# Performance work log

Hardware: AMD Instinct MI355X
Metric: run time of the kernel (lower is better)

## Reference

```python
import jax, jax.numpy as jnp
import numpy as np

B, S, D = 8, 2048, 512
EPS = float(jnp.finfo(jnp.float32).eps)  # torch RMSNorm eps=None -> finfo eps


def rmsnorm(x, w):
    var = jnp.mean(jnp.square(x), axis=-1, keepdims=True)
    return x * jax.lax.rsqrt(var + EPS) * w


def setup_inputs() -> dict:
    key = jax.random.key(0)
    ks = jax.random.split(key, 9)
    x = jax.random.normal(ks[0], (B, S, D), dtype=jnp.float32)
    q_expl = jax.random.normal(ks[1], (B, S, D), dtype=jnp.float32)
    k_expl = jax.random.normal(ks[2], (B, S, D), dtype=jnp.float32)
    # parameters (torch Linear: y = x @ W^T + b; store W already transposed [in, out])
    sc1 = 1.0 / np.sqrt(D)
    W1 = jax.random.uniform(ks[3], (D, 2 * D), jnp.float32, -sc1, sc1)
    b1 = jax.random.uniform(ks[4], (2 * D,), jnp.float32, -sc1, sc1)
    W2 = jax.random.uniform(ks[5], (D, D), jnp.float32, -sc1, sc1)
    b2 = jax.random.uniform(ks[6], (D,), jnp.float32, -sc1, sc1)
    norm1_w = jnp.ones((D,), jnp.float32)
    norm2_w = jnp.ones((D,), jnp.float32)
    return {"x": x, "q_expl": q_expl, "k_expl": k_expl,
            "W1": W1, "b1": b1, "W2": W2, "b2": b2,
            "norm1_w": norm1_w, "norm2_w": norm2_w}


def reference(x, q_expl, k_expl, W1, b1, W2, b2, norm1_w, norm2_w):
    d = x.shape[-1]
    # single-head attention: scores [B,S,S]
    scores = jnp.einsum('bqd,bkd->bqk', q_expl, k_expl) / jnp.sqrt(jnp.float32(d))
    attn = jax.nn.softmax(scores, axis=-1)
    attn_out = jnp.einsum('bqk,bkd->bqd', attn, x)
    # dropout is identity in eval mode
    h = rmsnorm(x + attn_out, norm1_w)
    # GeGLU FFN: Linear(D->2D), chunk, gelu(x1)*x2, Linear(D->D)
    proj = h @ W1 + b1
    x1, x2 = jnp.split(proj, 2, axis=-1)
    g = jax.nn.gelu(x1, approximate=False) * x2
    ff = g @ W2 + b2
    return rmsnorm(h + ff, norm2_w)
```

## Files before the change

kernel.cpp:

```cpp
#include <hip/hip_runtime.h>
#include <math.h>

static constexpr float EPS_F = 1.1920929e-07f;
static constexpr float SCL   = 0.044194173824159216f;

typedef __attribute__((ext_vector_type(8))) short  short8;
typedef __attribute__((ext_vector_type(4))) float  floatx4;

__device__ __forceinline__ float4 ld4(const float* p){ return *(const float4*)p; }
__device__ __forceinline__ ushort f2bf(float f){
  union { float f; unsigned u; } v; v.f = f;
  return (ushort)((v.u + 0x7FFFu + ((v.u >> 16) & 1u)) >> 16);
}
__device__ __forceinline__ float bf2f(ushort h){
  union { unsigned u; float f; } v; v.u = ((unsigned)h) << 16;
  return v.f;
}
#define MFMA16(A,B,C) __builtin_amdgcn_mfma_f32_16x16x32_bf16((A),(B),(C),0,0,0)

__device__ __forceinline__ void gld16(void* lds, const void* g){
  __builtin_amdgcn_global_load_lds(
      (const __attribute__((address_space(1))) unsigned int*)g,
      (__attribute__((address_space(3))) unsigned int*)lds, 16, 0, 0);
}


__global__ __launch_bounds__(256)
void cvt_qk(const float* __restrict__ q, const float* __restrict__ k,
            ushort* __restrict__ Qb, ushort* __restrict__ Kb)
{
  const size_t i4 = ((size_t)blockIdx.x*256 + threadIdx.x)*4;
  float4 v = ld4(q + i4);
  ushort4 o;
  o.x=f2bf(v.x*SCL); o.y=f2bf(v.y*SCL); o.z=f2bf(v.z*SCL); o.w=f2bf(v.w*SCL);
  *(ushort4*)(Qb + i4) = o;
  float4 u = ld4(k + i4);
  o.x=f2bf(u.x); o.y=f2bf(u.y); o.z=f2bf(u.z); o.w=f2bf(u.w);
  *(ushort4*)(Kb + i4) = o;
}

__global__ __launch_bounds__(256)
void transpose_cvt(const float* __restrict__ in, ushort* __restrict__ out,
                   int R, int C)
{
  __shared__ __align__(16) ushort tile[64*68];
  const int t = threadIdx.x;
  const size_t boff = (size_t)blockIdx.z * R * C;
  const int c0 = blockIdx.x*64, r0 = blockIdx.y*64;
#pragma unroll
  for (int it = 0; it < 4; ++it){
    int f = t + it*256, r = f >> 4, c4 = f & 15;
    float4 v = ld4(in + boff + (size_t)(r0+r)*C + c0 + c4*4);
    ushort4 o; o.x=f2bf(v.x); o.y=f2bf(v.y); o.z=f2bf(v.z); o.w=f2bf(v.w);
    *(ushort4*)&tile[r*68 + c4*4] = o;
  }
  __syncthreads();
#pragma unroll
  for (int it = 0; it < 4; ++it){
    int f = t + it*256, c = f >> 4, q4 = f & 15;
    ushort4 o;
    o.x = tile[(q4*4+0)*68 + c];
    o.y = tile[(q4*4+1)*68 + c];
    o.z = tile[(q4*4+2)*68 + c];
    o.w = tile[(q4*4+3)*68 + c];
    *(ushort4*)(out + boff + (size_t)(c0+c)*R + r0 + q4*4) = o;
  }
}

__global__ __launch_bounds__(256)
void qk_gemm(const ushort* __restrict__ Qbf, const ushort* __restrict__ Kbf,
             ushort* __restrict__ scores)
{
  __shared__ __align__(16) ushort As[128*32];
  __shared__ __align__(16) ushort Bs[128*32];
  const int t=threadIdx.x, lane=t&63, w=t>>6;
  const int b=blockIdx.z, m0=blockIdx.y*128, n0=blockIdx.x*128;
  const ushort* Qb = Qbf + ((size_t)b*2048 + m0)*512;
  const ushort* Kb = Kbf + ((size_t)b*2048 + n0)*512;
  const int sr = w*32 + (lane>>2);
  const int sc = (lane&3)*8;
  const int ga=(w&1)*4, gb2=(w>>1)*4;
  const int l15=lane&15, quad=lane>>4;

  floatx4 acc[4][4];
#pragma unroll
  for (int i=0;i<4;++i)
#pragma unroll
    for (int j=0;j<4;++j) acc[i][j]=(floatx4){0.f,0.f,0.f,0.f};

  for (int kc=0; kc<16; ++kc){
    const int k0 = kc*32;
    gld16(&As[(w*32)*32],    Qb + (size_t)sr*512      + k0 + sc);
    gld16(&As[(w*32+16)*32], Qb + (size_t)(sr+16)*512 + k0 + sc);
    gld16(&Bs[(w*32)*32],    Kb + (size_t)sr*512      + k0 + sc);
    gld16(&Bs[(w*32+16)*32], Kb + (size_t)(sr+16)*512 + k0 + sc);
    __syncthreads();
    short8 af[4], bfr[4];
#pragma unroll
    for (int i=0;i<4;++i) af[i]  = *(const short8*)&As[((ga+i)*16 + l15)*32 + quad*8];
#pragma unroll
    for (int j=0;j<4;++j) bfr[j] = *(const short8*)&Bs[((gb2+j)*16 + l15)*32 + quad*8];
#pragma unroll
    for (int i=0;i<4;++i)
#pragma unroll
      for (int j=0;j<4;++j)
        acc[i][j] = MFMA16(af[i], bfr[j], acc[i][j]);
    __syncthreads();
  }

  ushort* sb = scores + (size_t)b*2048*2048;
#pragma unroll
  for (int i=0;i<4;++i){
    const int rm = m0 + (ga+i)*16 + quad*4;
#pragma unroll
    for (int j=0;j<4;++j){
      const int cn = n0 + (gb2+j)*16 + l15;
#pragma unroll
      for (int r=0;r<4;++r)
        sb[(size_t)(rm+r)*2048 + cn] = f2bf(acc[i][j][r]);
    }
  }
}

__global__ __launch_bounds__(256)
void softmax_rows(ushort* __restrict__ sp)
{
  __shared__ float wred[8];
  const int t = threadIdx.x;
  ushort* row = sp + ((size_t)blockIdx.y*2048 + blockIdx.x)*2048;
  ushort4 u0 = *(const ushort4*)&row[t*4];
  ushort4 u1 = *(const ushort4*)&row[1024 + t*4];
  float v[8] = {bf2f(u0.x), bf2f(u0.y), bf2f(u0.z), bf2f(u0.w),
                bf2f(u1.x), bf2f(u1.y), bf2f(u1.z), bf2f(u1.w)};
  float mx = v[0];
#pragma unroll
  for (int e=1;e<8;++e) mx = fmaxf(mx, v[e]);
#pragma unroll
  for (int s=1;s<64;s<<=1) mx = fmaxf(mx, __shfl_xor(mx, s));
  if ((t&63)==0) wred[t>>6] = mx;
  __syncthreads();
  mx = fmaxf(fmaxf(wred[0],wred[1]), fmaxf(wred[2],wred[3]));
  float sum = 0.f;
#pragma unroll
  for (int e=0;e<8;++e){ v[e] = __expf(v[e]-mx); sum += v[e]; }
#pragma unroll
  for (int s=1;s<64;s<<=1) sum += __shfl_xor(sum, s);
  if ((t&63)==0) wred[4 + (t>>6)] = sum;
  __syncthreads();
  const float is = 1.0f/(wred[4]+wred[5]+wred[6]+wred[7]);
  u0.x=f2bf(v[0]*is); u0.y=f2bf(v[1]*is); u0.z=f2bf(v[2]*is); u0.w=f2bf(v[3]*is);
  u1.x=f2bf(v[4]*is); u1.y=f2bf(v[5]*is); u1.z=f2bf(v[6]*is); u1.w=f2bf(v[7]*is);
  *(ushort4*)&row[t*4] = u0;
  *(ushort4*)&row[1024 + t*4] = u1;
}

__global__ __launch_bounds__(512)
void pv_rms1(const ushort* __restrict__ P, const ushort* __restrict__ XT,
             const float* __restrict__ x, const float* __restrict__ n1w,
             ushort* __restrict__ hbf)
{
  __shared__ __align__(16) ushort Ps[64*32];
  __shared__ __align__(16) ushort Xs[512*32];
  __shared__ float red[64*8];
  const int t=threadIdx.x, lane=t&63, w=t>>6;
  const int m0=blockIdx.x*64, b=m0>>11, lm=m0&2047;
  const ushort* Pb = P  + ((size_t)b*2048 + lm)*2048;
  const ushort* Xb = XT + (size_t)b*512*2048;
  const int srq = lane>>2, sc=(lane&3)*8;
  const int l15=lane&15, quad=lane>>4;

  floatx4 acc[4][4];
#pragma unroll
  for (int i=0;i<4;++i)
#pragma unroll
    for (int j=0;j<4;++j) acc[i][j]=(floatx4){0.f,0.f,0.f,0.f};

  for (int kc=0; kc<64; ++kc){
    const int k0 = kc*32;
    if (w < 4)
      gld16(&Ps[(w*16)*32], Pb + (size_t)(w*16+srq)*2048 + k0 + sc);
#pragma unroll
    for (int i2=0;i2<4;++i2)
      gld16(&Xs[(w*64+i2*16)*32], Xb + (size_t)(w*64+i2*16+srq)*2048 + k0 + sc);
    __syncthreads();
    short8 af[4], bfr[4];
#pragma unroll
    for (int i=0;i<4;++i) af[i]  = *(const short8*)&Ps[(i*16 + l15)*32 + quad*8];
#pragma unroll
    for (int j=0;j<4;++j) bfr[j] = *(const short8*)&Xs[((w*4+j)*16 + l15)*32 + quad*8];
#pragma unroll
    for (int i=0;i<4;++i)
#pragma unroll
      for (int j=0;j<4;++j)
        acc[i][j] = MFMA16(af[i], bfr[j], acc[i][j]);
    __syncthreads();
  }

  float part[4][4];
#pragma unroll
  for (int i=0;i<4;++i)
#pragma unroll
    for (int r=0;r<4;++r) part[i][r]=0.f;
#pragma unroll
  for (int i=0;i<4;++i)
#pragma unroll
    for (int j=0;j<4;++j){
      const int col = w*64 + j*16 + l15;
#pragma unroll
      for (int r=0;r<4;++r){
        const int row = m0 + i*16 + quad*4 + r;
        float o = acc[i][j][r] + x[(size_t)row*512 + col];
        acc[i][j][r] = o;
        part[i][r] += o*o;
      }
    }
#pragma unroll
  for (int i=0;i<4;++i)
#pragma unroll
    for (int r=0;r<4;++r){
      float p = part[i][r];
      p += __shfl_xor(p,1); p += __shfl_xor(p,2);
      p += __shfl_xor(p,4); p += __shfl_xor(p,8);
      part[i][r] = p;
    }
  if (l15 == 0){
#pragma unroll
    for (int i=0;i<4;++i)
#pragma unroll
      for (int r=0;r<4;++r)
        red[(i*16 + quad*4 + r)*8 + w] = part[i][r];
  }
  __syncthreads();
#pragma unroll
  for (int i=0;i<4;++i)
#pragma unroll
    for (int r=0;r<4;++r){
      const int lr = i*16 + quad*4 + r;
      float tot = red[lr*8]+red[lr*8+1]+red[lr*8+2]+red[lr*8+3]
                + red[lr*8+4]+red[lr*8+5]+red[lr*8+6]+red[lr*8+7];
      part[i][r] = rsqrtf(tot*(1.0f/512.0f) + EPS_F);
    }
#pragma unroll
  for (int i=0;i<4;++i)
#pragma unroll
    for (int j=0;j<4;++j){
      const int col = w*64 + j*16 + l15;
      const float wv = n1w[col];
#pragma unroll
      for (int r=0;r<4;++r){
        const int row = m0 + i*16 + quad*4 + r;
        hbf[(size_t)row*512 + col] = f2bf(acc[i][j][r] * part[i][r] * wv);
      }
    }
}

__global__ __launch_bounds__(256)
void ffn1(const ushort* __restrict__ hbf, const ushort* __restrict__ W1T,
          const float* __restrict__ b1, ushort* __restrict__ gbuf)
{
  __shared__ __align__(16) ushort As[128*32];
  __shared__ __align__(16) ushort Bs[128*32];
  const int t=threadIdx.x, lane=t&63, w=t>>6;
  const int n0=blockIdx.x*64, m0=blockIdx.y*128;
  const int sr = w*32 + (lane>>2), sc=(lane&3)*8;
  const int ga=(w&1)*4, b2=(w>>1);
  const int l15=lane&15, quad=lane>>4;
  const int gr0 = (sr < 64) ? (n0+sr) : (448+n0+sr);
  const int sr1 = sr+16;
  const int gr1 = (sr1 < 64) ? (n0+sr1) : (448+n0+sr1);

  floatx4 acc[4][4];
#pragma unroll
  for (int i=0;i<4;++i)
#pragma unroll
    for (int j=0;j<4;++j) acc[i][j]=(floatx4){0.f,0.f,0.f,0.f};

  for (int kc=0; kc<16; ++kc){
    const int k0 = kc*32;
    gld16(&As[(w*32)*32],    hbf + (size_t)(m0+sr)*512  + k0 + sc);
    gld16(&As[(w*32+16)*32], hbf + (size_t)(m0+sr1)*512 + k0 + sc);
    gld16(&Bs[(w*32)*32],    W1T + (size_t)gr0*512 + k0 + sc);
    gld16(&Bs[(w*32+16)*32], W1T + (size_t)gr1*512 + k0 + sc);
    __syncthreads();
    short8 af[4], bfr[4];
#pragma unroll
    for (int i=0;i<4;++i) af[i] = *(const short8*)&As[((ga+i)*16 + l15)*32 + quad*8];
#pragma unroll
    for (int jj=0;jj<4;++jj){
      const int g1 = (jj<2) ? (b2*2+jj) : (4 + b2*2 + (jj-2));
      bfr[jj] = *(const short8*)&Bs[(g1*16 + l15)*32 + quad*8];
    }
#pragma unroll
    for (int i=0;i<4;++i)
#pragma unroll
      for (int jj=0;jj<4;++jj)
        acc[i][jj] = MFMA16(af[i], bfr[jj], acc[i][jj]);
    __syncthreads();
  }

#pragma unroll
  for (int i=0;i<4;++i){
#pragma unroll
    for (int jj=0;jj<2;++jj){
      const int col = n0 + (b2*2+jj)*16 + l15;
      const float bb1 = b1[col], bb2 = b1[512+col];
#pragma unroll
      for (int r=0;r<4;++r){
        const int row = m0 + (ga+i)*16 + quad*4 + r;
        float x1 = acc[i][jj][r]   + bb1;
        float x2 = acc[i][jj+2][r] + bb2;
        float gl = 0.5f*x1*(1.0f + erff(x1*0.70710678118654752f));
        gbuf[(size_t)row*512 + col] = f2bf(gl*x2);
      }
    }
  }
}

__global__ __launch_bounds__(512)
void ffn2_rms2(const ushort* __restrict__ gb, const ushort* __restrict__ W2T,
               const float* __restrict__ b2, const ushort* __restrict__ hbf,
               const float* __restrict__ n2w, float* __restrict__ out)
{
  __shared__ __align__(16) ushort As[64*32];
  __shared__ __align__(16) ushort Bs[512*32];
  __shared__ float red[64*8];
  const int t=threadIdx.x, lane=t&63, w=t>>6;
  const int m0=blockIdx.x*64;
  const int srq = lane>>2, sc=(lane&3)*8;
  const int l15=lane&15, quad=lane>>4;

  floatx4 acc[4][4];
#pragma unroll
  for (int i=0;i<4;++i)
#pragma unroll
    for (int j=0;j<4;++j) acc[i][j]=(floatx4){0.f,0.f,0.f,0.f};

  for (int kc=0; kc<16; ++kc){
    const int k0 = kc*32;
    if (w < 4)
      gld16(&As[(w*16)*32], gb + (size_t)(m0+w*16+srq)*512 + k0 + sc);
#pragma unroll
    for (int i2=0;i2<4;++i2)
      gld16(&Bs[(w*64+i2*16)*32], W2T + (size_t)(w*64+i2*16+srq)*512 + k0 + sc);
    __syncthreads();
    short8 af[4], bfr[4];
#pragma unroll
    for (int i=0;i<4;++i) af[i]  = *(const short8*)&As[(i*16 + l15)*32 + quad*8];
#pragma unroll
    for (int j=0;j<4;++j) bfr[j] = *(const short8*)&Bs[((w*4+j)*16 + l15)*32 + quad*8];
#pragma unroll
    for (int i=0;i<4;++i)
#pragma unroll
      for (int j=0;j<4;++j)
        acc[i][j] = MFMA16(af[i], bfr[j], acc[i][j]);
    __syncthreads();
  }

  float part[4][4];
#pragma unroll
  for (int i=0;i<4;++i)
#pragma unroll
    for (int r=0;r<4;++r) part[i][r]=0.f;
#pragma unroll
  for (int i=0;i<4;++i)
#pragma unroll
    for (int j=0;j<4;++j){
      const int col = w*64 + j*16 + l15;
      const float bb = b2[col];
#pragma unroll
      for (int r=0;r<4;++r){
        const int row = m0 + i*16 + quad*4 + r;
        float y = acc[i][j][r] + bb + bf2f(hbf[(size_t)row*512 + col]);
        acc[i][j][r] = y;
        part[i][r] += y*y;
      }
    }
#pragma unroll
  for (int i=0;i<4;++i)
#pragma unroll
    for (int r=0;r<4;++r){
      float p = part[i][r];
      p += __shfl_xor(p,1); p += __shfl_xor(p,2);
      p += __shfl_xor(p,4); p += __shfl_xor(p,8);
      part[i][r] = p;
    }
  if (l15 == 0){
#pragma unroll
    for (int i=0;i<4;++i)
#pragma unroll
      for (int r=0;r<4;++r)
        red[(i*16 + quad*4 + r)*8 + w] = part[i][r];
  }
  __syncthreads();
#pragma unroll
  for (int i=0;i<4;++i)
#pragma unroll
    for (int r=0;r<4;++r){
      const int lr = i*16 + quad*4 + r;
      float tot = red[lr*8]+red[lr*8+1]+red[lr*8+2]+red[lr*8+3]
                + red[lr*8+4]+red[lr*8+5]+red[lr*8+6]+red[lr*8+7];
      part[i][r] = rsqrtf(tot*(1.0f/512.0f) + EPS_F);
    }
#pragma unroll
  for (int i=0;i<4;++i)
#pragma unroll
    for (int j=0;j<4;++j){
      const int col = w*64 + j*16 + l15;
      const float wv = n2w[col];
#pragma unroll
      for (int r=0;r<4;++r){
        const int row = m0 + i*16 + quad*4 + r;
        out[(size_t)row*512 + col] = acc[i][j][r] * part[i][r] * wv;
      }
    }
}

extern "C" void kernel_launch(void* const* d_in, const int* in_sizes, int n_in,
                              void* d_out, int out_size, void* d_ws, size_t ws_size,
                              hipStream_t stream)
{
  const float* x   = (const float*)d_in[0];
  const float* q   = (const float*)d_in[1];
  const float* k   = (const float*)d_in[2];
  const float* W1  = (const float*)d_in[3];
  const float* b1  = (const float*)d_in[4];
  const float* W2  = (const float*)d_in[5];
  const float* b2  = (const float*)d_in[6];
  const float* n1w = (const float*)d_in[7];
  const float* n2w = (const float*)d_in[8];
  float* out = (float*)d_out;

  ushort* scoresP = (ushort*)d_ws;
  ushort* XT  = scoresP + (size_t)8*2048*2048;
  ushort* Qbf = XT  + (size_t)8*512*2048;
  ushort* Kbf = Qbf + (size_t)8*2048*512;
  ushort* W1T = Kbf + (size_t)8*2048*512;
  ushort* W2T = W1T + (size_t)1024*512;
  ushort* hbf  = Qbf;
  ushort* gbuf = Kbf;

  cvt_qk       <<<dim3(8192),     256, 0, stream>>>(q, k, Qbf, Kbf);
  transpose_cvt<<<dim3(8, 32, 8), 256, 0, stream>>>(x,  XT,  2048, 512);
  transpose_cvt<<<dim3(16, 8, 1), 256, 0, stream>>>(W1, W1T, 512, 1024);
  transpose_cvt<<<dim3(8,  8, 1), 256, 0, stream>>>(W2, W2T, 512, 512);

  qk_gemm      <<<dim3(16, 16, 8), 256, 0, stream>>>(Qbf, Kbf, scoresP);
  softmax_rows <<<dim3(2048, 8),   256, 0, stream>>>(scoresP);
  pv_rms1      <<<dim3(256),       512, 0, stream>>>(scoresP, XT, x, n1w, hbf);
  ffn1         <<<dim3(8, 128),    256, 0, stream>>>(hbf, W1T, b1, gbuf);
  ffn2_rms2    <<<dim3(256),       512, 0, stream>>>(gbuf, W2T, b2, hbf, n2w, out);
}
```

Baseline: 365.4 us.

## Double-buffer LDS in all GEMM kernels and halve row tiles for PV/FFN2

```diff
diff --git a/kernel.cpp b/kernel.cpp
--- a/kernel.cpp
+++ b/kernel.cpp
@@ -71,16 +71,14 @@
 void qk_gemm(const ushort* __restrict__ Qbf, const ushort* __restrict__ Kbf,
              ushort* __restrict__ scores)
 {
-  __shared__ __align__(16) ushort As[128*32];
-  __shared__ __align__(16) ushort Bs[128*32];
+  __shared__ __align__(16) ushort As[2][128*32];
+  __shared__ __align__(16) ushort Bs[2][128*32];
   const int t=threadIdx.x, lane=t&63, w=t>>6;
   const int b=blockIdx.z, m0=blockIdx.y*128, n0=blockIdx.x*128;
   const ushort* Qb = Qbf + ((size_t)b*2048 + m0)*512;
   const ushort* Kb = Kbf + ((size_t)b*2048 + n0)*512;
-  const int sr = w*32 + (lane>>2);
-  const int sc = (lane&3)*8;
-  const int ga=(w&1)*4, gb2=(w>>1)*4;
-  const int l15=lane&15, quad=lane>>4;
+  const int sr = w*32 + (lane>>2), sc = (lane&3)*8;
+  const int ga=(w&1)*4, gb2=(w>>1)*4, l15=lane&15, quad=lane>>4;
 
   floatx4 acc[4][4];
 #pragma unroll
@@ -88,24 +86,29 @@
 #pragma unroll
     for (int j=0;j<4;++j) acc[i][j]=(floatx4){0.f,0.f,0.f,0.f};
 
+  auto stage = [&](int buf, int k0){
+    gld16(&As[buf][(w*32)*32],    Qb + (size_t)sr*512      + k0 + sc);
+    gld16(&As[buf][(w*32+16)*32], Qb + (size_t)(sr+16)*512 + k0 + sc);
+    gld16(&Bs[buf][(w*32)*32],    Kb + (size_t)sr*512      + k0 + sc);
+    gld16(&Bs[buf][(w*32+16)*32], Kb + (size_t)(sr+16)*512 + k0 + sc);
+  };
+
+  stage(0, 0);
   for (int kc=0; kc<16; ++kc){
-    const int k0 = kc*32;
-    gld16(&As[(w*32)*32],    Qb + (size_t)sr*512      + k0 + sc);
-    gld16(&As[(w*32+16)*32], Qb + (size_t)(sr+16)*512 + k0 + sc);
-    gld16(&Bs[(w*32)*32],    Kb + (size_t)sr*512      + k0 + sc);
-    gld16(&Bs[(w*32+16)*32], Kb + (size_t)(sr+16)*512 + k0 + sc);
     __syncthreads();
+    if (kc < 15) stage((kc+1)&1, (kc+1)*32);
+    const ushort* A = As[kc&1];
+    const ushort* B = Bs[kc&1];
     short8 af[4], bfr[4];
 #pragma unroll
-    for (int i=0;i<4;++i) af[i]  = *(const short8*)&As[((ga+i)*16 + l15)*32 + quad*8];
-#pragma unroll
-    for (int j=0;j<4;++j) bfr[j] = *(const short8*)&Bs[((gb2+j)*16 + l15)*32 + quad*8];
+    for (int i=0;i<4;++i) af[i]  = *(const short8*)&A[((ga+i)*16 + l15)*32 + quad*8];
+#pragma unroll
+    for (int j=0;j<4;++j) bfr[j] = *(const short8*)&B[((gb2+j)*16 + l15)*32 + quad*8];
 #pragma unroll
     for (int i=0;i<4;++i)
 #pragma unroll
       for (int j=0;j<4;++j)
         acc[i][j] = MFMA16(af[i], bfr[j], acc[i][j]);
-    __syncthreads();
   }
 
   ushort* sb = scores + (size_t)b*2048*2048;
@@ -159,50 +162,55 @@
              const float* __restrict__ x, const float* __restrict__ n1w,
              ushort* __restrict__ hbf)
 {
-  __shared__ __align__(16) ushort Ps[64*32];
-  __shared__ __align__(16) ushort Xs[512*32];
-  __shared__ float red[64*8];
+  __shared__ __align__(16) ushort Ps[2][32*32];
+  __shared__ __align__(16) ushort Xs[2][512*32];
+  __shared__ float red[32*8];
   const int t=threadIdx.x, lane=t&63, w=t>>6;
-  const int m0=blockIdx.x*64, b=m0>>11, lm=m0&2047;
+  const int m0=blockIdx.x*32, b=m0>>11, lm=m0&2047;
   const ushort* Pb = P  + ((size_t)b*2048 + lm)*2048;
   const ushort* Xb = XT + (size_t)b*512*2048;
   const int srq = lane>>2, sc=(lane&3)*8;
   const int l15=lane&15, quad=lane>>4;
 
-  floatx4 acc[4][4];
-#pragma unroll
-  for (int i=0;i<4;++i)
+  floatx4 acc[2][4];
+#pragma unroll
+  for (int i=0;i<2;++i)
 #pragma unroll
     for (int j=0;j<4;++j) acc[i][j]=(floatx4){0.f,0.f,0.f,0.f};
 
+  auto stage = [&](int buf, int k0){
+    if (w < 2)
+      gld16(&Ps[buf][(w*16)*32], Pb + (size_t)(w*16+srq)*2048 + k0 + sc);
+#pragma unroll
+    for (int i2=0;i2<4;++i2)
+      gld16(&Xs[buf][(w*64+i2*16)*32], Xb + (size_t)(w*64+i2*16+srq)*2048 + k0 + sc);
+  };
+
+  stage(0, 0);
   for (int kc=0; kc<64; ++kc){
-    const int k0 = kc*32;
-    if (w < 4)
-      gld16(&Ps[(w*16)*32], Pb + (size_t)(w*16+srq)*2048 + k0 + sc);
-#pragma unroll
-    for (int i2=0;i2<4;++i2)
-      gld16(&Xs[(w*64+i2*16)*32], Xb + (size_t)(w*64+i2*16+srq)*2048 + k0 + sc);
     __syncthreads();
-    short8 af[4], bfr[4];
-#pragma unroll
-    for (int i=0;i<4;++i) af[i]  = *(const short8*)&Ps[(i*16 + l15)*32 + quad*8];
-#pragma unroll
-    for (int j=0;j<4;++j) bfr[j] = *(const short8*)&Xs[((w*4+j)*16 + l15)*32 + quad*8];
-#pragma unroll
-    for (int i=0;i<4;++i)
+    if (kc < 63) stage((kc+1)&1, (kc+1)*32);
+    const ushort* A = Ps[kc&1];
+    const ushort* B = Xs[kc&1];
+    short8 af[2], bfr[4];
+#pragma unroll
+    for (int i=0;i<2;++i) af[i]  = *(const short8*)&A[(i*16 + l15)*32 + quad*8];
+#pragma unroll
+    for (int j=0;j<4;++j) bfr[j] = *(const short8*)&B[((w*4+j)*16 + l15)*32 + quad*8];
+#pragma unroll
+    for (int i=0;i<2;++i)
 #pragma unroll
       for (int j=0;j<4;++j)
         acc[i][j] = MFMA16(af[i], bfr[j], acc[i][j]);
-    __syncthreads();
-  }
-
-  float part[4][4];
-#pragma unroll
-  for (int i=0;i<4;++i)
+  }
+
+  float part[2][4];
+#pragma unroll
+  for (int i=0;i<2;++i)
 #pragma unroll
     for (int r=0;r<4;++r) part[i][r]=0.f;
 #pragma unroll
-  for (int i=0;i<4;++i)
+  for (int i=0;i<2;++i)
 #pragma unroll
     for (int j=0;j<4;++j){
       const int col = w*64 + j*16 + l15;
@@ -215,7 +223,7 @@
       }
     }
 #pragma unroll
-  for (int i=0;i<4;++i)
+  for (int i=0;i<2;++i)
 #pragma unroll
     for (int r=0;r<4;++r){
       float p = part[i][r];
@@ -225,14 +233,14 @@
     }
   if (l15 == 0){
 #pragma unroll
-    for (int i=0;i<4;++i)
+    for (int i=0;i<2;++i)
 #pragma unroll
       for (int r=0;r<4;++r)
         red[(i*16 + quad*4 + r)*8 + w] = part[i][r];
   }
   __syncthreads();
 #pragma unroll
-  for (int i=0;i<4;++i)
+  for (int i=0;i<2;++i)
 #pragma unroll
     for (int r=0;r<4;++r){
       const int lr = i*16 + quad*4 + r;
@@ -241,7 +249,7 @@
       part[i][r] = rsqrtf(tot*(1.0f/512.0f) + EPS_F);
     }
 #pragma unroll
-  for (int i=0;i<4;++i)
+  for (int i=0;i<2;++i)
 #pragma unroll
     for (int j=0;j<4;++j){
       const int col = w*64 + j*16 + l15;
@@ -258,12 +266,12 @@
 void ffn1(const ushort* __restrict__ hbf, const ushort* __restrict__ W1T,
           const float* __restrict__ b1, ushort* __restrict__ gbuf)
 {
-  __shared__ __align__(16) ushort As[128*32];
-  __shared__ __align__(16) ushort Bs[128*32];
+  __shared__ __align__(16) ushort As[2][128*32];
+  __shared__ __align__(16) ushort Bs[2][128*32];
   const int t=threadIdx.x, lane=t&63, w=t>>6;
   const int n0=blockIdx.x*64, m0=blockIdx.y*128;
   const int sr = w*32 + (lane>>2), sc=(lane&3)*8;
-  const int ga=(w&1)*4, b2=(w>>1);
+  const int ga=(w&1)*4, b2w=(w>>1);
   const int l15=lane&15, quad=lane>>4;
   const int gr0 = (sr < 64) ? (n0+sr) : (448+n0+sr);
   const int sr1 = sr+16;
@@ -275,34 +283,39 @@
 #pragma unroll
     for (int j=0;j<4;++j) acc[i][j]=(floatx4){0.f,0.f,0.f,0.f};
 
+  auto stage = [&](int buf, int k0){
+    gld16(&As[buf][(w*32)*32],    hbf + (size_t)(m0+sr)*512  + k0 + sc);
+    gld16(&As[buf][(w*32+16)*32], hbf + (size_t)(m0+sr1)*512 + k0 + sc);
+    gld16(&Bs[buf][(w*32)*32],    W1T + (size_t)gr0*512 + k0 + sc);
+    gld16(&Bs[buf][(w*32+16)*32], W1T + (size_t)gr1*512 + k0 + sc);
+  };
+
+  stage(0, 0);
   for (int kc=0; kc<16; ++kc){
-    const int k0 = kc*32;
-    gld16(&As[(w*32)*32],    hbf + (size_t)(m0+sr)*512  + k0 + sc);
-    gld16(&As[(w*32+16)*32], hbf + (size_t)(m0+sr1)*512 + k0 + sc);
-    gld16(&Bs[(w*32)*32],    W1T + (size_t)gr0*512 + k0 + sc);
-    gld16(&Bs[(w*32+16)*32], W1T + (size_t)gr1*512 + k0 + sc);
     __syncthreads();
+    if (kc < 15) stage((kc+1)&1, (kc+1)*32);
+    const ushort* A = As[kc&1];
+    const ushort* B = Bs[kc&1];
     short8 af[4], bfr[4];
 #pragma unroll
-    for (int i=0;i<4;++i) af[i] = *(const short8*)&As[((ga+i)*16 + l15)*32 + quad*8];
+    for (int i=0;i<4;++i) af[i] = *(const short8*)&A[((ga+i)*16 + l15)*32 + quad*8];
 #pragma unroll
     for (int jj=0;jj<4;++jj){
-      const int g1 = (jj<2) ? (b2*2+jj) : (4 + b2*2 + (jj-2));
-      bfr[jj] = *(const short8*)&Bs[(g1*16 + l15)*32 + quad*8];
+      const int g1 = (jj<2) ? (b2w*2+jj) : (4 + b2w*2 + (jj-2));
+      bfr[jj] = *(const short8*)&B[(g1*16 + l15)*32 + quad*8];
     }
 #pragma unroll
     for (int i=0;i<4;++i)
 #pragma unroll
       for (int jj=0;jj<4;++jj)
         acc[i][jj] = MFMA16(af[i], bfr[jj], acc[i][jj]);
-    __syncthreads();
   }
 
 #pragma unroll
   for (int i=0;i<4;++i){
 #pragma unroll
     for (int jj=0;jj<2;++jj){
-      const int col = n0 + (b2*2+jj)*16 + l15;
+      const int col = n0 + (b2w*2+jj)*16 + l15;
       const float bb1 = b1[col], bb2 = b1[512+col];
 #pragma unroll
       for (int r=0;r<4;++r){
@@ -321,48 +334,53 @@
                const float* __restrict__ b2, const ushort* __restrict__ hbf,
                const float* __restrict__ n2w, float* __restrict__ out)
 {
-  __shared__ __align__(16) ushort As[64*32];
-  __shared__ __align__(16) ushort Bs[512*32];
-  __shared__ float red[64*8];
+  __shared__ __align__(16) ushort As[2][32*32];
+  __shared__ __align__(16) ushort Bs[2][512*32];
+  __shared__ float red[32*8];
   const int t=threadIdx.x, lane=t&63, w=t>>6;
-  const int m0=blockIdx.x*64;
+  const int m0=blockIdx.x*32;
   const int srq = lane>>2, sc=(lane&3)*8;
   const int l15=lane&15, quad=lane>>4;
 
-  floatx4 acc[4][4];
-#pragma unroll
-  for (int i=0;i<4;++i)
+  floatx4 acc[2][4];
+#pragma unroll
+  for (int i=0;i<2;++i)
 #pragma unroll
     for (int j=0;j<4;++j) acc[i][j]=(floatx4){0.f,0.f,0.f,0.f};
 
+  auto stage = [&](int buf, int k0){
+    if (w < 2)
+      gld16(&As[buf][(w*16)*32], gb + (size_t)(m0+w*16+srq)*512 + k0 + sc);
+#pragma unroll
+    for (int i2=0;i2<4;++i2)
+      gld16(&Bs[buf][(w*64+i2*16)*32], W2T + (size_t)(w*64+i2*16+srq)*512 + k0 + sc);
+  };
+
+  stage(0, 0);
   for (int kc=0; kc<16; ++kc){
-    const int k0 = kc*32;
-    if (w < 4)
-      gld16(&As[(w*16)*32], gb + (size_t)(m0+w*16+srq)*512 + k0 + sc);
-#pragma unroll
-    for (int i2=0;i2<4;++i2)
-      gld16(&Bs[(w*64+i2*16)*32], W2T + (size_t)(w*64+i2*16+srq)*512 + k0 + sc);
     __syncthreads();
-    short8 af[4], bfr[4];
-#pragma unroll
-    for (int i=0;i<4;++i) af[i]  = *(const short8*)&As[(i*16 + l15)*32 + quad*8];
-#pragma unroll
-    for (int j=0;j<4;++j) bfr[j] = *(const short8*)&Bs[((w*4+j)*16 + l15)*32 + quad*8];
-#pragma unroll
-    for (int i=0;i<4;++i)
+    if (kc < 15) stage((kc+1)&1, (kc+1)*32);
+    const ushort* A = As[kc&1];
+    const ushort* B = Bs[kc&1];
+    short8 af[2], bfr[4];
+#pragma unroll
+    for (int i=0;i<2;++i) af[i]  = *(const short8*)&A[(i*16 + l15)*32 + quad*8];
+#pragma unroll
+    for (int j=0;j<4;++j) bfr[j] = *(const short8*)&B[((w*4+j)*16 + l15)*32 + quad*8];
+#pragma unroll
+    for (int i=0;i<2;++i)
 #pragma unroll
       for (int j=0;j<4;++j)
         acc[i][j] = MFMA16(af[i], bfr[j], acc[i][j]);
-    __syncthreads();
-  }
-
-  float part[4][4];
-#pragma unroll
-  for (int i=0;i<4;++i)
+  }
+
+  float part[2][4];
+#pragma unroll
+  for (int i=0;i<2;++i)
 #pragma unroll
     for (int r=0;r<4;++r) part[i][r]=0.f;
 #pragma unroll
-  for (int i=0;i<4;++i)
+  for (int i=0;i<2;++i)
 #pragma unroll
     for (int j=0;j<4;++j){
       const int col = w*64 + j*16 + l15;
@@ -376,7 +394,7 @@
       }
     }
 #pragma unroll
-  for (int i=0;i<4;++i)
+  for (int i=0;i<2;++i)
 #pragma unroll
     for (int r=0;r<4;++r){
       float p = part[i][r];
@@ -386,14 +404,14 @@
     }
   if (l15 == 0){
 #pragma unroll
-    for (int i=0;i<4;++i)
+    for (int i=0;i<2;++i)
 #pragma unroll
       for (int r=0;r<4;++r)
         red[(i*16 + quad*4 + r)*8 + w] = part[i][r];
   }
   __syncthreads();
 #pragma unroll
-  for (int i=0;i<4;++i)
+  for (int i=0;i<2;++i)
 #pragma unroll
     for (int r=0;r<4;++r){
       const int lr = i*16 + quad*4 + r;
@@ -402,7 +420,7 @@
       part[i][r] = rsqrtf(tot*(1.0f/512.0f) + EPS_F);
     }
 #pragma unroll
-  for (int i=0;i<4;++i)
+  for (int i=0;i<2;++i)
 #pragma unroll
     for (int j=0;j<4;++j){
       const int col = w*64 + j*16 + l15;
@@ -446,7 +464,7 @@
 
   qk_gemm      <<<dim3(16, 16, 8), 256, 0, stream>>>(Qbf, Kbf, scoresP);
   softmax_rows <<<dim3(2048, 8),   256, 0, stream>>>(scoresP);
-  pv_rms1      <<<dim3(256),       512, 0, stream>>>(scoresP, XT, x, n1w, hbf);
+  pv_rms1      <<<dim3(512),       512, 0, stream>>>(scoresP, XT, x, n1w, hbf);
   ffn1         <<<dim3(8, 128),    256, 0, stream>>>(hbf, W1T, b1, gbuf);
-  ffn2_rms2    <<<dim3(256),       512, 0, stream>>>(gbuf, W2T, b2, hbf, n2w, out);
-}
+  ffn2_rms2    <<<dim3(512),       512, 0, stream>>>(gbuf, W2T, b2, hbf, n2w, out);
+}
```

After: 375.4 us. 2.7% more time.
